# Performance work log

Measured on AMD Instinct MI355X. Metric: run time of the kernel, lower is better.

The kernel has to match this reference:

```python
import jax, jax.numpy as jnp
import numpy as np

B, L, D, H, E, M, P = 2, 512, 768, 12, 32, 4, 256
EMB, BS, MAP, C = 768, 64, 256, 97


def setup_inputs() -> dict:
    key = jax.random.key(0)
    ks = jax.random.split(key, 16)
    w = lambda k, s: (0.02 * jax.random.normal(k, s, jnp.float32))
    seq = jax.random.normal(ks[0], (B, L, D), jnp.float32)
    attn = jax.random.uniform(ks[1], (B, H, L, L), jnp.float32)
    entity_pos = jax.random.randint(ks[2], (B, E, M), 0, L - 2)
    # distinct (h, t) entity pairs per document -> unique mention-pair scatter slots
    grid = jnp.stack(jnp.meshgrid(jnp.arange(E), jnp.arange(E), indexing='ij'), -1).reshape(-1, 2)
    hts = jnp.stack([grid[jax.random.permutation(jax.random.fold_in(ks[3], b), E * E)[:P]] for b in range(B)], 0)
    mention_idx = jnp.broadcast_to(jnp.arange(E * M).reshape(E, M), (B, E, M))
    return {
        'seq': seq, 'attn': attn,
        'entity_pos': entity_pos, 'hts': hts, 'mention_idx': mention_idx,
        'W_head': w(ks[4], (2 * D, EMB)), 'b_head': jnp.zeros((EMB,), jnp.float32),
        'W_tail': w(ks[5], (2 * D, EMB)), 'b_tail': jnp.zeros((EMB,), jnp.float32),
        'W_rel': w(ks[6], (EMB * BS, C)), 'b_rel': jnp.zeros((C,), jnp.float32),
        'W_fh': w(ks[7], (D, EMB)), 'W_ft': w(ks[8], (D, EMB)), 'b_f': jnp.zeros((EMB,), jnp.float32),
        'W_unet': w(ks[9], (EMB, C)), 'b_unet': jnp.zeros((C,), jnp.float32),
        'W_mlp': w(ks[10], (EMB, C)), 'b_mlp': jnp.zeros((C,), jnp.float32),
        'W_bil': w(ks[11], (3 * C, C)), 'b_bil': jnp.zeros((C,), jnp.float32),
    }


def reference(seq, attn, entity_pos, hts, mention_idx,
              W_head, b_head, W_tail, b_tail, W_rel, b_rel,
              W_fh, W_ft, b_f, W_unet, b_unet, W_mlp, b_mlp, W_bil, b_bil):
    pos = entity_pos + 1                                 # bert offset
    b3 = jnp.arange(B)[:, None, None]
    ment_emb = seq[b3, pos]                              # [B,E,M,D] mention gather
    ment_att = attn[b3, :, pos]                          # [B,E,M,H,L]
    ent_emb = jax.nn.logsumexp(ment_emb, axis=2)         # [B,E,D] logsumexp pool
    ent_att = ment_att.mean(axis=2)                      # [B,E,H,L]
    b2 = jnp.arange(B)[:, None]
    h_idx, t_idx = hts[..., 0], hts[..., 1]
    hs, ts = ent_emb[b2, h_idx], ent_emb[b2, t_idx]      # [B,P,D]
    ha, ta = ent_att[b2, h_idx], ent_att[b2, t_idx]      # [B,P,H,L]
    ht_att = (ha * ta).mean(2)                           # [B,P,L]
    ht_att = ht_att / (ht_att.sum(-1, keepdims=True) + 1e-5)
    rs = jnp.einsum('bld,bpl->bpd', seq, ht_att)         # localized context
    N = B * P
    hz = jnp.tanh(jnp.concatenate([hs, rs], -1).reshape(N, 2 * D) @ W_head + b_head)
    tz = jnp.tanh(jnp.concatenate([ts, rs], -1).reshape(N, 2 * D) @ W_tail + b_tail)
    bl = (hz.reshape(N, EMB // BS, BS, 1) * tz.reshape(N, EMB // BS, 1, BS)).reshape(N, EMB * BS)
    r1 = bl @ W_rel + b_rel                              # [N,C]
    # mention-pair dense map scatter (map_rss)
    ment_flat = ment_emb.reshape(B, E * M, D)
    mh = mention_idx[b2, h_idx]                          # [B,P,M]
    mt = mention_idx[b2, t_idx]
    mh2 = jnp.broadcast_to(mh[:, :, :, None], (B, P, M, M))
    mt2 = jnp.broadcast_to(mt[:, :, None, :], (B, P, M, M))
    b4 = jnp.broadcast_to(jnp.arange(B)[:, None, None, None], (B, P, M, M))
    eh = ment_flat[b4, mh2]                              # [B,P,M,M,D]
    et = ment_flat[b4, mt2]
    feat = eh @ W_fh + et @ W_ft + b_f                   # fused Linear(cat(h,t))
    mp = jnp.zeros((B, MAP, MAP, EMB), seq.dtype).at[b4, mh2, mt2].set(feat)
    enc2 = jnp.tanh(mp @ W_unet + b_unet)                # UNet-channel surrogate
    enc3 = jax.nn.gelu(mp @ W_mlp + b_mlp)               # MLP-channel surrogate
    r2 = jax.nn.logsumexp(enc2[b4, mh2, mt2], axis=(2, 3)).reshape(N, C)
    r3 = jax.nn.logsumexp(enc3[b4, mh2, mt2], axis=(2, 3)).reshape(N, C)
    return jnp.concatenate([r1, r2, r3], -1) @ W_bil + b_bil
```

## Files before the change

kernel.cpp:

```cpp
#include <hip/hip_runtime.h>
#include <hip/hip_bf16.h>

#define B_  2
#define L_  512
#define D_  768
#define H_  12
#define E_  32
#define M_  4
#define P_  256
#define EMB_ 768
#define BS_ 64
#define C_  97
#define N_  (B_*P_)

#define KTOT_    49152
#define CPAD_    112
#define KSPLIT_  48
#define KCHUNK_  (KTOT_/KSPLIT_)
#define PSTR_    128
#define TILE_    (CPAD_*64)

typedef __hip_bfloat16 bf16;
typedef __attribute__((ext_vector_type(8))) short bf16x8;
typedef __attribute__((ext_vector_type(4))) float f32x4;
typedef __attribute__((ext_vector_type(8))) float f32x8;

__device__ inline float ldIn(const void* p, long idx, int isbf) {
    return isbf ? (float)((const bf16*)p)[idx] : ((const float*)p)[idx];
}

__device__ inline unsigned short f2bf(float f) {
    bf16 h = (bf16)f;
    return *(unsigned short*)&h;
}

__device__ inline float bf2f(unsigned short u) {
    bf16 h = *(bf16*)&u;
    return (float)h;
}

__global__ void dtype_detect(const void* __restrict__ seq, int* __restrict__ flag,
                             float* __restrict__ c23) {
    __shared__ int cnt;
    if (threadIdx.x == 0) cnt = 0;
    if (threadIdx.x < 2*C_) c23[threadIdx.x] = 0.f;
    __syncthreads();
    const unsigned short* u = (const unsigned short*)seq;
    int bad = 0;
    for (int i = threadIdx.x; i < 1024; i += 256) {
        unsigned short e = (u[i] >> 7) & 0xFF;
        if (e >= 140) bad++;
    }
    atomicAdd(&cnt, bad);
    __syncthreads();
    if (threadIdx.x == 0) flag[0] = (cnt < 16) ? 1 : 0;
}

struct PrepArgs {
    const void* src[8];
    long off[8];
    int K[8];
    int Ncols[8];
    int Npad[8];
    unsigned short* dst[8];
    const void* W_bil;  float* W_bilF;
    const void* b_f; const void* W_unet; const void* b_unet;
    const void* W_mlp; const void* b_mlp; float* c23;
    const void* W_rel; unsigned short* WBt;
};

union PrepSm {
    float T[32][65];
    unsigned short TW[CPAD_][72];
};

__global__ void prep_kernel(PrepArgs a, const int* __restrict__ dtf) {
    int isbf = dtf[0];
    int z = blockIdx.z;
    __shared__ PrepSm sm;
    int tid = threadIdx.x;
    if (z == 0) {
        int lin = blockIdx.y*48 + blockIdx.x;
        if (lin >= 96) return;
        int c = tid;
        if (c >= C_) return;
        float s2 = 0.f, s3 = 0.f;
        int d0 = lin*8;
        for (int i = 0; i < 8; i++) {
            int d = d0 + i;
            float bf = ldIn(a.b_f, d, isbf);
            s2 += bf * ldIn(a.W_unet, (long)d*C_ + c, isbf);
            s3 += bf * ldIn(a.W_mlp,  (long)d*C_ + c, isbf);
        }
        if (lin == 0) {
            s2 += ldIn(a.b_unet, c, isbf);
            s3 += ldIn(a.b_mlp,  c, isbf);
        }
        atomicAdd(&a.c23[c], s2);
        atomicAdd(&a.c23[C_ + c], s3);
    } else if (z == 1) {
        int lin = blockIdx.y*48 + blockIdx.x;
        if (lin >= KTOT_/64) return;
        int k0 = lin * 64;
        for (int idx = tid; idx < 64*97; idx += 256) {
            int kk = idx / 97, c = idx % 97;
            sm.TW[c][kk] = f2bf(ldIn(a.W_rel, (long)(k0+kk)*C_ + c, isbf));
        }
        for (int idx = tid; idx < 15*64; idx += 256) {
            sm.TW[97 + (idx>>6)][idx & 63] = 0;
        }
        __syncthreads();
        unsigned short* tb = a.WBt + (long)lin*TILE_;
        for (int t = 0; t < 4; t++) {
            int idx = tid + t*256;
            if (idx < 896) {
                int l  = idx & 63;
                int h  = (idx >> 6) & 1;
                int ct = idx >> 7;
                int row = ct*16 + (l & 15);
                int col = h*32 + (l >> 4)*8;
                *(uint4*)(tb + idx*8) = *(uint4*)&sm.TW[row][col];
            }
        }
    } else if (z <= 9) {
        int j = z - 2;
        int K = a.K[j], Ncols = a.Ncols[j], Npad = a.Npad[j];
        int k0 = blockIdx.x*32, n0 = blockIdx.y*64;
        if (k0 >= K || n0 >= Npad) return;
        const void* src = a.src[j];
        long off = a.off[j];
        unsigned short* dst = a.dst[j];
        int c64 = tid & 63, r4 = tid >> 6;
        for (int p = 0; p < 8; p++) {
            int r = r4 + p*4;
            int n = n0 + c64;
            sm.T[r][c64] = (n < Ncols) ? ldIn(src, off + (long)(k0+r)*Ncols + n, isbf) : 0.f;
        }
        __syncthreads();
        int cc = tid & 31, n8 = tid >> 5;
        for (int p = 0; p < 8; p++) {
            int nn = n8 + p*8;
            dst[(long)(n0+nn)*K + k0 + cc] = f2bf(sm.T[cc][nn]);
        }
    } else {
        int lin = blockIdx.y*48 + blockIdx.x;
        int idx = lin*256 + tid;
        if (idx < 291*C_) a.W_bilF[idx] = ldIn(a.W_bil, idx, isbf);
    }
}

__global__ void gather_kernel(const void* __restrict__ seq, const void* __restrict__ attn,
                              const int* __restrict__ entity_pos,
                              unsigned short* __restrict__ mentb, float* __restrict__ ent_emb,
                              float* __restrict__ ent_att, const int* __restrict__ dtf) {
    int isbf = dtf[0];
    if (blockIdx.x < 768) {
        int beh = blockIdx.x;
        int h = beh % H_;
        int be = beh / H_;
        int b = be >> 5;
        int pos[M_];
        for (int m = 0; m < M_; m++) pos[m] = entity_pos[be*M_+m] + 1;
        for (int l = threadIdx.x; l < L_; l += 256) {
            float s = 0.f;
            for (int m = 0; m < M_; m++)
                s += ldIn(attn, (((long)(b*H_ + h))*L_ + pos[m])*L_ + l, isbf);
            ent_att[(long)beh*L_ + l] = 0.25f * s;
        }
    } else {
        int be = blockIdx.x - 768;
        int b = be >> 5;
        int pos[M_];
        for (int m = 0; m < M_; m++) pos[m] = entity_pos[be*M_+m] + 1;
        for (int d = threadIdx.x; d < D_; d += 256) {
            float x[M_];
            for (int m = 0; m < M_; m++) {
                x[m] = ldIn(seq, ((long)b*L_ + pos[m])*D_ + d, isbf);
                mentb[((long)be*M_ + m)*D_ + d] = f2bf(x[m]);
            }
            float mx = fmaxf(fmaxf(x[0],x[1]), fmaxf(x[2],x[3]));
            float s = expf(x[0]-mx)+expf(x[1]-mx)+expf(x[2]-mx)+expf(x[3]-mx);
            ent_emb[(long)be*D_ + d] = mx + logf(s);
        }
    }
}

__global__ void htatt_kernel(const float* __restrict__ ent_att, const int* __restrict__ hts,
                             unsigned short* __restrict__ htb) {
    int bp = blockIdx.x;
    int b = bp >> 8;
    int h_e = hts[bp*2+0], t_e = hts[bp*2+1];
    const float* ea_h = ent_att + (long)((b*E_ + h_e)*H_)*L_;
    const float* ea_t = ent_att + (long)((b*E_ + t_e)*H_)*L_;
    __shared__ float red[256];
    float v[2];
    for (int t = 0; t < 2; t++) {
        int l = threadIdx.x + t*256;
        float s = 0.f;
        for (int h = 0; h < H_; h++) s += ea_h[h*L_+l] * ea_t[h*L_+l];
        v[t] = s * (1.0f/H_);
    }
    red[threadIdx.x] = v[0] + v[1];
    __syncthreads();
    for (int off = 128; off > 0; off >>= 1) {
        if (threadIdx.x < off) red[threadIdx.x] += red[threadIdx.x+off];
        __syncthreads();
    }
    float inv = 1.0f / (red[0] + 1e-5f);
    for (int t = 0; t < 2; t++) {
        int l = threadIdx.x + t*256;
        htb[(long)bp*L_ + l] = f2bf(v[t] * inv);
    }
}

__global__ void catb_kernel(const float* __restrict__ ent_emb, const float* __restrict__ rs,
                            const int* __restrict__ hts,
                            unsigned short* __restrict__ hcatb, unsigned short* __restrict__ tcatb) {
    int n = blockIdx.x;
    int b = n >> 8;
    int h_e = hts[n*2+0], t_e = hts[n*2+1];
    const float* eh = ent_emb + (long)(b*E_ + h_e)*D_;
    const float* et = ent_emb + (long)(b*E_ + t_e)*D_;
    const float* r  = rs + (long)n*D_;
    for (int k = threadIdx.x; k < D_; k += 256) {
        hcatb[(long)n*1536 + k] = f2bf(eh[k]);
        tcatb[(long)n*1536 + k] = f2bf(et[k]);
        unsigned short rb = f2bf(r[k]);
        hcatb[(long)n*1536 + 768 + k] = rb;
        tcatb[(long)n*1536 + 768 + k] = rb;
    }
}

struct MfmaJob {
    const unsigned short* A[4];
    const unsigned short* Bt[4];
    const void* bias[4];
    void* C[4];
    int K[4];
    int ldc[4];
    int act[4];
    int obf[4];
};

__global__ void mfma_nt2_kernel(MfmaJob args, const int* __restrict__ dtf) {
    int z = blockIdx.z;
    const unsigned short* A  = args.A[z];
    const unsigned short* Bt = args.Bt[z];
    const void* bias = args.bias[z];
    void* C = args.C[z];
    int K = args.K[z], ldc = args.ldc[z], act = args.act[z], obf = args.obf[z];
    __shared__ unsigned short Al[2][32][72];
    __shared__ unsigned short Btl[2][32][72];
    int m0 = blockIdx.x*32, n0 = blockIdx.y*32;
    int tid = threadIdx.x, wave = tid>>6, lane = tid&63;
    int lm = lane&15, lq = lane>>4;
    int rowg = wave>>1, cgrp = wave&1;
    int rr = tid >> 3;
    int kc = (tid & 7) * 8;
    uint4 ra, rb;

    ra = *(const uint4*)(A  + (long)(m0+rr)*K + kc);
    rb = *(const uint4*)(Bt + (long)(n0+rr)*K + kc);
    *(uint4*)&Al[0][rr][kc]  = ra;
    *(uint4*)&Btl[0][rr][kc] = rb;

    int nst = K >> 6;
    f32x4 acc = {};
    for (int ks = 0; ks < nst; ks++) {
        __syncthreads();
        if (ks+1 < nst) {
            int k0 = (ks+1) << 6;
            ra = *(const uint4*)(A  + (long)(m0+rr)*K + k0 + kc);
            rb = *(const uint4*)(Bt + (long)(n0+rr)*K + k0 + kc);
        }
        int cb = ks & 1;
        #pragma unroll
        for (int half = 0; half < 2; half++) {
            bf16x8 af  = *(bf16x8*)&Al[cb][rowg*16+lm][half*32+lq*8];
            bf16x8 bfr = *(bf16x8*)&Btl[cb][cgrp*16+lm][half*32+lq*8];
            acc = __builtin_amdgcn_mfma_f32_16x16x32_bf16(af, bfr, acc, 0, 0, 0);
        }
        if (ks+1 < nst) {
            int nb = (ks+1) & 1;
            *(uint4*)&Al[nb][rr][kc]  = ra;
            *(uint4*)&Btl[nb][rr][kc] = rb;
        }
    }
    int isbf = dtf[0];
    int n = n0 + cgrp*16 + lm;
    float bia = bias ? ldIn(bias, n, isbf) : 0.f;
    #pragma unroll
    for (int r = 0; r < 4; r++) {
        int m = m0 + rowg*16 + lq*4 + r;
        float v = acc[r] + bia;
        if (act == 1) v = tanhf(v);
        if (obf) ((unsigned short*)C)[(long)m*ldc + n] = f2bf(v);
        else     ((float*)C)[(long)m*ldc + n] = v;
    }
}

__global__ __launch_bounds__(256, 3)
void r1_mfma_kernel(const float* __restrict__ hz, const float* __restrict__ tz,
                    const unsigned short* __restrict__ WBt,
                    float* __restrict__ partial) {
    __shared__ float hzL[32][17];
    int kz = blockIdx.x;
    int nb0 = blockIdx.y * 32;
    int gk0 = kz * 16;
    int gi0 = kz * 16;
    int g0 = (kz * KCHUNK_) >> 12;
    int tid = threadIdx.x;
    int wave = tid >> 6, lane = tid & 63;
    int lm = lane & 15;
    int ctb = wave * 2;
    int nct = (wave < 3) ? 2 : 1;

    {
        int r = tid >> 3, q = (tid & 7) * 2;
        float2 v = *(const float2*)(hz + (long)(nb0 + r)*EMB_ + gi0 + q);
        hzL[r][q] = v.x; hzL[r][q+1] = v.y;
    }
    int lq = lane >> 4;
    f32x8 tza[2], tzb[2];
    #pragma unroll
    for (int rg = 0; rg < 2; rg++) {
        const float* tp = tz + (long)(nb0 + rg*16 + lm)*EMB_ + g0*64;
        float4 x0 = *(const float4*)(tp + lq*8);
        float4 y0 = *(const float4*)(tp + lq*8 + 4);
        float4 x1 = *(const float4*)(tp + 32 + lq*8);
        float4 y1 = *(const float4*)(tp + 32 + lq*8 + 4);
        tza[rg][0]=x0.x; tza[rg][1]=x0.y; tza[rg][2]=x0.z; tza[rg][3]=x0.w;
        tza[rg][4]=y0.x; tza[rg][5]=y0.y; tza[rg][6]=y0.z; tza[rg][7]=y0.w;
        tzb[rg][0]=x1.x; tzb[rg][1]=x1.y; tzb[rg][2]=x1.z; tzb[rg][3]=x1.w;
        tzb[rg][4]=y1.x; tzb[rg][5]=y1.y; tzb[rg][6]=y1.z; tzb[rg][7]=y1.w;
    }
    __syncthreads();

    const unsigned short* wb = WBt + (long)gk0*TILE_ + lane*8;

    f32x4 acc[2][2] = {};
    bf16x8 cb[2][2];
    #pragma unroll
    for (int ct = 0; ct < 2; ct++)
        if (ct < nct)
            #pragma unroll
            for (int h = 0; h < 2; h++)
                cb[ct][h] = *(const bf16x8*)(wb + ((ctb+ct)*2 + h)*512);

    #pragma unroll 2
    for (int ks = 0; ks < KCHUNK_/64; ks++) {
        bf16x8 nbuf[2][2];
        if (ks+1 < KCHUNK_/64) {
            const unsigned short* wn = wb + (long)(ks+1)*TILE_;
            #pragma unroll
            for (int ct = 0; ct < 2; ct++)
                if (ct < nct)
                    #pragma unroll
                    for (int h = 0; h < 2; h++)
                        nbuf[ct][h] = *(const bf16x8*)(wn + ((ctb+ct)*2 + h)*512);
        }
        float hv0 = hzL[lm][ks];
        float hv1 = hzL[16 + lm][ks];
        unsigned short o00[8], o01[8], o10[8], o11[8];
        #pragma unroll
        for (int e = 0; e < 8; e++) {
            o00[e] = f2bf(tza[0][e] * hv0);
            o01[e] = f2bf(tzb[0][e] * hv0);
            o10[e] = f2bf(tza[1][e] * hv1);
            o11[e] = f2bf(tzb[1][e] * hv1);
        }
        bf16x8 a00 = *(bf16x8*)o00, a01 = *(bf16x8*)o01;
        bf16x8 a10 = *(bf16x8*)o10, a11 = *(bf16x8*)o11;
        #pragma unroll
        for (int ct = 0; ct < 2; ct++) {
            if (ct < nct) {
                acc[ct][0] = __builtin_amdgcn_mfma_f32_16x16x32_bf16(a00, cb[ct][0], acc[ct][0], 0, 0, 0);
                acc[ct][0] = __builtin_amdgcn_mfma_f32_16x16x32_bf16(a01, cb[ct][1], acc[ct][0], 0, 0, 0);
                acc[ct][1] = __builtin_amdgcn_mfma_f32_16x16x32_bf16(a10, cb[ct][0], acc[ct][1], 0, 0, 0);
                acc[ct][1] = __builtin_amdgcn_mfma_f32_16x16x32_bf16(a11, cb[ct][1], acc[ct][1], 0, 0, 0);
            }
        }
        if (ks+1 < KCHUNK_/64) {
            #pragma unroll
            for (int ct = 0; ct < 2; ct++)
                if (ct < nct)
                    #pragma unroll
                    for (int h = 0; h < 2; h++)
                        cb[ct][h] = nbuf[ct][h];
        }
    }
    #pragma unroll
    for (int ct = 0; ct < 2; ct++) {
        if (ct < nct || wave == 3) {
            int c = (ctb + ct)*16 + lm;
            #pragma unroll
            for (int rg = 0; rg < 2; rg++) {
                #pragma unroll
                for (int r = 0; r < 4; r++) {
                    int nl = rg*16 + lq*4 + r;
                    float v = (ct < nct) ? acc[ct][rg][r] : 0.f;
                    partial[((long)(nb0+nl)*KSPLIT_ + kz)*PSTR_ + c] = v;
                }
            }
        }
    }
}

__global__ void r23out_kernel(const float* __restrict__ partial, const void* __restrict__ b_rel,
                              const float* __restrict__ mu, const float* __restrict__ c23,
                              const int* __restrict__ hts, const int* __restrict__ mention_idx,
                              const float* __restrict__ W_bilF, const void* __restrict__ b_bil,
                              void* __restrict__ out, const int* __restrict__ dtf) {
    int bp = blockIdx.x;
    int b = bp >> 8;
    int c = threadIdx.x;
    int isbf = dtf[0];
    __shared__ float row[292];
    if (c < C_) {
        const float* pr = partial + (long)bp*KSPLIT_*PSTR_;
        float r1v = 0.f;
        #pragma unroll 8
        for (int kz = 0; kz < KSPLIT_; kz++)
            r1v += pr[kz*PSTR_ + c];
        r1v += ldIn(b_rel, c, isbf);
        int h_e = hts[bp*2+0], t_e = hts[bp*2+1];
        const float* mu2h = mu;
        const float* mu2t = mu + 32768;
        const float* mu3h = mu + 65536;
        const float* mu3t = mu + 98304;
        float ah2[4], at2[4], ah3[4], at3[4];
        for (int m = 0; m < 4; m++) {
            int emh = mention_idx[(b*E_ + h_e)*M_ + m];
            int emt = mention_idx[(b*E_ + t_e)*M_ + m];
            ah2[m] = mu2h[(long)(b*128 + emh)*128 + c];
            ah3[m] = mu3h[(long)(b*128 + emh)*128 + c];
            at2[m] = mu2t[(long)(b*128 + emt)*128 + c];
            at3[m] = mu3t[(long)(b*128 + emt)*128 + c];
        }
        float c2 = c23[c], c3 = c23[C_ + c];
        float v2[16], v3[16];
        int q = 0;
        for (int i = 0; i < 4; i++) {
            for (int j = 0; j < 4; j++, q++) {
                float x2 = ah2[i] + at2[j] + c2;
                v2[q] = tanhf(x2);
                float x3 = ah3[i] + at3[j] + c3;
                float t = tanhf(0.7978845608028654f * (x3 + 0.044715f*x3*x3*x3));
                v3[q] = 0.5f * x3 * (1.0f + t);
            }
        }
        float m2 = v2[0], m3 = v3[0];
        for (q = 1; q < 16; q++) { m2 = fmaxf(m2, v2[q]); m3 = fmaxf(m3, v3[q]); }
        float s2 = 0.f, s3 = 0.f;
        for (q = 0; q < 16; q++) { s2 += expf(v2[q]-m2); s3 += expf(v3[q]-m3); }
        row[c]        = r1v;
        row[C_ + c]   = m2 + logf(s2);
        row[2*C_ + c] = m3 + logf(s3);
    }
    __syncthreads();
    if (c >= C_) return;
    float a0 = 0.f, a1 = 0.f, a2 = 0.f, a3 = 0.f;
    #pragma unroll 4
    for (int k = 0; k < 288; k += 4) {
        a0 += row[k+0] * W_bilF[(k+0)*C_ + c];
        a1 += row[k+1] * W_bilF[(k+1)*C_ + c];
        a2 += row[k+2] * W_bilF[(k+2)*C_ + c];
        a3 += row[k+3] * W_bilF[(k+3)*C_ + c];
    }
    a0 += row[288] * W_bilF[288*C_ + c];
    a1 += row[289] * W_bilF[289*C_ + c];
    a2 += row[290] * W_bilF[290*C_ + c];
    float v = a0 + a1 + a2 + a3 + ldIn(b_bil, c, isbf);
    if (isbf) ((bf16*)out)[(long)bp*C_ + c] = (bf16)v;
    else      ((float*)out)[(long)bp*C_ + c] = v;
}

extern "C" void kernel_launch(void* const* d_in, const int* in_sizes, int n_in,
                              void* d_out, int out_size, void* d_ws, size_t ws_size,
                              hipStream_t stream) {
    const void* seq        = d_in[0];
    const void* attn       = d_in[1];
    const int*  entity_pos = (const int*)d_in[2];
    const int*  hts        = (const int*)d_in[3];
    const int*  mention_idx= (const int*)d_in[4];
    const void* W_head     = d_in[5];
    const void* b_head     = d_in[6];
    const void* W_tail     = d_in[7];
    const void* b_tail     = d_in[8];
    const void* W_rel      = d_in[9];
    const void* b_rel      = d_in[10];
    const void* W_fh       = d_in[11];
    const void* W_ft       = d_in[12];
    const void* b_f        = d_in[13];
    const void* W_unet     = d_in[14];
    const void* b_unet     = d_in[15];
    const void* W_mlp      = d_in[16];
    const void* b_mlp      = d_in[17];
    const void* W_bil      = d_in[18];
    const void* b_bil      = d_in[19];

    float* w = (float*)d_ws;
    int*   dtf      = (int*)w;
    unsigned short* mentb = (unsigned short*)(w + 64);
    float* ent_emb  = w + 98368;
    float* ent_att  = w + 147520;
    unsigned short* htb = (unsigned short*)(w + 540736);
    float* rs       = w + 671808;
    float* hz       = w + 1065024;
    float* tz       = w + 1458240;
    float* mu       = w + 1851456;
    float* c23      = w + 1982528;
    unsigned short* seqT  = (unsigned short*)(w + 1982784);
    unsigned short* WhT   = (unsigned short*)(w + 2376000);
    unsigned short* WtT   = (unsigned short*)(w + 2965824);
    unsigned short* WfhT  = (unsigned short*)(w + 3555648);
    unsigned short* WftT  = (unsigned short*)(w + 3850560);
    unsigned short* WunetT= (unsigned short*)(w + 4145472);
    unsigned short* WmlpT = (unsigned short*)(w + 4194624);
    unsigned short* Tbh   = (unsigned short*)(w + 4243776);
    unsigned short* Tbt   = (unsigned short*)(w + 4342080);
    unsigned short* hcatb = (unsigned short*)(w + 4440384);
    unsigned short* tcatb = (unsigned short*)(w + 4833600);
    unsigned short* WBt   = (unsigned short*)(w + 5226816);
    float* partial  = w + 7979328;
    float* W_bilF   = w + 11649344;

    dtype_detect<<<1, 256, 0, stream>>>(seq, dtf, c23);
    {
        PrepArgs a = {};
        const void* srcs[8] = {W_head, W_tail, W_fh, W_ft, W_unet, W_mlp, seq, seq};
        long offs[8]   = {0,0,0,0,0,0,0,393216};
        int Ks[8]      = {1536,1536,768,768,768,768,512,512};
        int Ncols8[8]  = {768,768,768,768,97,97,768,768};
        int Npads[8]   = {768,768,768,768,128,128,768,768};
        unsigned short* dsts[8] = {WhT, WtT, WfhT, WftT, WunetT, WmlpT, seqT, seqT+393216};
        for (int z = 0; z < 8; z++) {
            a.src[z]=srcs[z]; a.off[z]=offs[z]; a.K[z]=Ks[z];
            a.Ncols[z]=Ncols8[z]; a.Npad[z]=Npads[z]; a.dst[z]=dsts[z];
        }
        a.W_bil = W_bil; a.W_bilF = W_bilF;
        a.b_f = b_f; a.W_unet = W_unet; a.b_unet = b_unet;
        a.W_mlp = W_mlp; a.b_mlp = b_mlp; a.c23 = c23;
        a.W_rel = W_rel; a.WBt = WBt;
        prep_kernel<<<dim3(48, 16, 11), 256, 0, stream>>>(a, dtf);
    }
    gather_kernel<<<768 + 64, 256, 0, stream>>>(seq, attn, entity_pos, mentb, ent_emb, ent_att, dtf);
    htatt_kernel<<<N_, 256, 0, stream>>>(ent_att, hts, htb);
    {
        MfmaJob ga = {};
        for (int z = 0; z < 2; z++) {
            ga.A[z] = htb + (long)z*256*512; ga.Bt[z] = seqT + (long)z*393216;
            ga.bias[z] = nullptr; ga.C[z] = rs + (long)z*256*768;
            ga.K[z] = 512; ga.ldc[z] = 768; ga.act[z] = 0; ga.obf[z] = 0;
        }
        ga.A[2] = mentb; ga.Bt[2] = WfhT; ga.bias[2] = nullptr; ga.C[2] = Tbh;
        ga.K[2] = 768; ga.ldc[2] = 768; ga.act[2] = 0; ga.obf[2] = 1;
        ga.A[3] = mentb; ga.Bt[3] = WftT; ga.bias[3] = nullptr; ga.C[3] = Tbt;
        ga.K[3] = 768; ga.ldc[3] = 768; ga.act[3] = 0; ga.obf[3] = 1;
        mfma_nt2_kernel<<<dim3(8, 24, 4), 256, 0, stream>>>(ga, dtf);
    }
    catb_kernel<<<N_, 256, 0, stream>>>(ent_emb, rs, hts, hcatb, tcatb);
    {
        MfmaJob ga = {};
        ga.A[0] = hcatb; ga.Bt[0] = WhT; ga.bias[0] = b_head; ga.C[0] = hz;
        ga.A[1] = tcatb; ga.Bt[1] = WtT; ga.bias[1] = b_tail; ga.C[1] = tz;
        for (int z = 0; z < 2; z++) { ga.K[z] = 1536; ga.ldc[z] = 768; ga.act[z] = 1; ga.obf[z] = 0; }
        mfma_nt2_kernel<<<dim3(16, 24, 2), 256, 0, stream>>>(ga, dtf);
    }
    {
        MfmaJob ga = {};
        const unsigned short* As[4] = {Tbh, Tbt, Tbh, Tbt};
        const unsigned short* Bs[4] = {WunetT, WunetT, WmlpT, WmlpT};
        for (int q = 0; q < 4; q++) {
            ga.A[q] = As[q]; ga.Bt[q] = Bs[q]; ga.bias[q] = nullptr;
            ga.C[q] = mu + q*32768;
            ga.K[q] = 768; ga.ldc[q] = 128; ga.act[q] = 0; ga.obf[q] = 0;
        }
        mfma_nt2_kernel<<<dim3(8, 4, 4), 256, 0, stream>>>(ga, dtf);
    }
    r1_mfma_kernel<<<dim3(KSPLIT_, 16), 256, 0, stream>>>(hz, tz, WBt, partial);
    r23out_kernel<<<N_, 128, 0, stream>>>(partial, b_rel, mu, c23, hts, mention_idx,
                                          W_bilF, b_bil, d_out, dtf);
}
```

Measured before the change: 218.0 us.

## Fuse dtype detection, entity attention and pair attention; merge small GEMM launches

Drops the separate dtype_detect kernel; each kernel now detects dtype inline with a wave ballot over the first 64 elements of seq. The entity attention averaging and the head/tail attention product are fused into one kernel that reads attn rows directly per pair, so the ent_att intermediate goes away. The c23 bias reduction now writes 16 partials instead of using atomics, which also removes the need to zero the buffer first. The two trailing small GEMM launches are merged into one launch with per-job bounds. This removes launches and intermediate traffic but recomputes attention gathers per pair, and the dtype check now samples fewer elements.

```diff
diff --git a/kernel.cpp b/kernel.cpp
--- a/kernel.cpp
+++ b/kernel.cpp
@@ -34,26 +34,12 @@
     return *(unsigned short*)&h;
 }
 
-__device__ inline float bf2f(unsigned short u) {
-    bf16 h = *(bf16*)&u;
-    return (float)h;
-}
-
-__global__ void dtype_detect(const void* __restrict__ seq, int* __restrict__ flag,
-                             float* __restrict__ c23) {
-    __shared__ int cnt;
-    if (threadIdx.x == 0) cnt = 0;
-    if (threadIdx.x < 2*C_) c23[threadIdx.x] = 0.f;
-    __syncthreads();
-    const unsigned short* u = (const unsigned short*)seq;
-    int bad = 0;
-    for (int i = threadIdx.x; i < 1024; i += 256) {
-        unsigned short e = (u[i] >> 7) & 0xFF;
-        if (e >= 140) bad++;
-    }
-    atomicAdd(&cnt, bad);
-    __syncthreads();
-    if (threadIdx.x == 0) flag[0] = (cnt < 16) ? 1 : 0;
+__device__ inline int detect_bf(const void* seqd) {
+    const unsigned short* u = (const unsigned short*)seqd;
+    int lane = threadIdx.x & 63;
+    unsigned short e = (u[lane] >> 7) & 0xFF;
+    unsigned long long m = __ballot(e >= 140);
+    return m == 0ull;
 }
 
 struct PrepArgs {
@@ -65,8 +51,9 @@
     unsigned short* dst[8];
     const void* W_bil;  float* W_bilF;
     const void* b_f; const void* W_unet; const void* b_unet;
-    const void* W_mlp; const void* b_mlp; float* c23;
+    const void* W_mlp; const void* b_mlp; float* c23p;
     const void* W_rel; unsigned short* WBt;
+    const void* seqd;
 };
 
 union PrepSm {
@@ -74,19 +61,19 @@
     unsigned short TW[CPAD_][72];
 };
 
-__global__ void prep_kernel(PrepArgs a, const int* __restrict__ dtf) {
-    int isbf = dtf[0];
+__global__ void prep_kernel(PrepArgs a) {
+    int isbf = detect_bf(a.seqd);
     int z = blockIdx.z;
     __shared__ PrepSm sm;
     int tid = threadIdx.x;
     if (z == 0) {
         int lin = blockIdx.y*48 + blockIdx.x;
-        if (lin >= 96) return;
+        if (lin >= 16) return;
         int c = tid;
         if (c >= C_) return;
         float s2 = 0.f, s3 = 0.f;
-        int d0 = lin*8;
-        for (int i = 0; i < 8; i++) {
+        int d0 = lin*48;
+        for (int i = 0; i < 48; i++) {
             int d = d0 + i;
             float bf = ldIn(a.b_f, d, isbf);
             s2 += bf * ldIn(a.W_unet, (long)d*C_ + c, isbf);
@@ -96,8 +83,8 @@
             s2 += ldIn(a.b_unet, c, isbf);
             s3 += ldIn(a.b_mlp,  c, isbf);
         }
-        atomicAdd(&a.c23[c], s2);
-        atomicAdd(&a.c23[C_ + c], s3);
+        a.c23p[lin*194 + c]      = s2;
+        a.c23p[lin*194 + 97 + c] = s3;
     } else if (z == 1) {
         int lin = blockIdx.y*48 + blockIdx.x;
         if (lin >= KTOT_/64) return;
@@ -149,26 +136,49 @@
     }
 }
 
-__global__ void gather_kernel(const void* __restrict__ seq, const void* __restrict__ attn,
-                              const int* __restrict__ entity_pos,
-                              unsigned short* __restrict__ mentb, float* __restrict__ ent_emb,
-                              float* __restrict__ ent_att, const int* __restrict__ dtf) {
-    int isbf = dtf[0];
-    if (blockIdx.x < 768) {
-        int beh = blockIdx.x;
-        int h = beh % H_;
-        int be = beh / H_;
-        int b = be >> 5;
-        int pos[M_];
-        for (int m = 0; m < M_; m++) pos[m] = entity_pos[be*M_+m] + 1;
-        for (int l = threadIdx.x; l < L_; l += 256) {
+__global__ void ghatt_kernel(const void* __restrict__ seq, const void* __restrict__ attn,
+                             const int* __restrict__ entity_pos, const int* __restrict__ hts,
+                             unsigned short* __restrict__ mentb, float* __restrict__ ent_emb,
+                             unsigned short* __restrict__ htb) {
+    int isbf = detect_bf(seq);
+    if (blockIdx.x < 512) {
+        int bp = blockIdx.x;
+        int b = bp >> 8;
+        int h_e = hts[bp*2+0], t_e = hts[bp*2+1];
+        int ph[M_], pt[M_];
+        for (int m = 0; m < M_; m++) {
+            ph[m] = entity_pos[(b*E_ + h_e)*M_ + m] + 1;
+            pt[m] = entity_pos[(b*E_ + t_e)*M_ + m] + 1;
+        }
+        __shared__ float red[256];
+        float v[2];
+        for (int t = 0; t < 2; t++) {
+            int l = threadIdx.x + t*256;
             float s = 0.f;
-            for (int m = 0; m < M_; m++)
-                s += ldIn(attn, (((long)(b*H_ + h))*L_ + pos[m])*L_ + l, isbf);
-            ent_att[(long)beh*L_ + l] = 0.25f * s;
+            for (int h = 0; h < H_; h++) {
+                long hb = ((long)(b*H_ + h))*L_;
+                float ha = 0.f, ta = 0.f;
+                for (int m = 0; m < M_; m++) {
+                    ha += ldIn(attn, (hb + ph[m])*L_ + l, isbf);
+                    ta += ldIn(attn, (hb + pt[m])*L_ + l, isbf);
+                }
+                s += ha * ta;
+            }
+            v[t] = s * (0.0625f / H_);
+        }
+        red[threadIdx.x] = v[0] + v[1];
+        __syncthreads();
+        for (int off = 128; off > 0; off >>= 1) {
+            if (threadIdx.x < off) red[threadIdx.x] += red[threadIdx.x+off];
+            __syncthreads();
+        }
+        float inv = 1.0f / (red[0] + 1e-5f);
+        for (int t = 0; t < 2; t++) {
+            int l = threadIdx.x + t*256;
+            htb[(long)bp*L_ + l] = f2bf(v[t] * inv);
         }
     } else {
-        int be = blockIdx.x - 768;
+        int be = blockIdx.x - 512;
         int b = be >> 5;
         int pos[M_];
         for (int m = 0; m < M_; m++) pos[m] = entity_pos[be*M_+m] + 1;
@@ -182,34 +192,6 @@
             float s = expf(x[0]-mx)+expf(x[1]-mx)+expf(x[2]-mx)+expf(x[3]-mx);
             ent_emb[(long)be*D_ + d] = mx + logf(s);
         }
-    }
-}
-
-__global__ void htatt_kernel(const float* __restrict__ ent_att, const int* __restrict__ hts,
-                             unsigned short* __restrict__ htb) {
-    int bp = blockIdx.x;
-    int b = bp >> 8;
-    int h_e = hts[bp*2+0], t_e = hts[bp*2+1];
-    const float* ea_h = ent_att + (long)((b*E_ + h_e)*H_)*L_;
-    const float* ea_t = ent_att + (long)((b*E_ + t_e)*H_)*L_;
-    __shared__ float red[256];
-    float v[2];
-    for (int t = 0; t < 2; t++) {
-        int l = threadIdx.x + t*256;
-        float s = 0.f;
-        for (int h = 0; h < H_; h++) s += ea_h[h*L_+l] * ea_t[h*L_+l];
-        v[t] = s * (1.0f/H_);
-    }
-    red[threadIdx.x] = v[0] + v[1];
-    __syncthreads();
-    for (int off = 128; off > 0; off >>= 1) {
-        if (threadIdx.x < off) red[threadIdx.x] += red[threadIdx.x+off];
-        __syncthreads();
-    }
-    float inv = 1.0f / (red[0] + 1e-5f);
-    for (int t = 0; t < 2; t++) {
-        int l = threadIdx.x + t*256;
-        htb[(long)bp*L_ + l] = f2bf(v[t] * inv);
     }
 }
 
@@ -232,18 +214,24 @@
 }
 
 struct MfmaJob {
-    const unsigned short* A[4];
-    const unsigned short* Bt[4];
-    const void* bias[4];
-    void* C[4];
-    int K[4];
-    int ldc[4];
-    int act[4];
-    int obf[4];
+    const unsigned short* A[8];
+    const unsigned short* Bt[8];
+    const void* bias[8];
+    void* C[8];
+    const void* seqd;
+    int K[8];
+    int ldc[8];
+    int act[8];
+    int obf[8];
+    int Mt[8];
+    int Nt[8];
 };
 
-__global__ void mfma_nt2_kernel(MfmaJob args, const int* __restrict__ dtf) {
+__global__ void mfma_nt2_kernel(MfmaJob args) {
     int z = blockIdx.z;
+    int m0 = blockIdx.x*32, n0 = blockIdx.y*32;
+    if (m0 >= args.Mt[z] || n0 >= args.Nt[z]) return;
+    int isbf = detect_bf(args.seqd);
     const unsigned short* A  = args.A[z];
     const unsigned short* Bt = args.Bt[z];
     const void* bias = args.bias[z];
@@ -251,7 +239,6 @@
     int K = args.K[z], ldc = args.ldc[z], act = args.act[z], obf = args.obf[z];
     __shared__ unsigned short Al[2][32][72];
     __shared__ unsigned short Btl[2][32][72];
-    int m0 = blockIdx.x*32, n0 = blockIdx.y*32;
     int tid = threadIdx.x, wave = tid>>6, lane = tid&63;
     int lm = lane&15, lq = lane>>4;
     int rowg = wave>>1, cgrp = wave&1;
@@ -286,7 +273,6 @@
             *(uint4*)&Btl[nb][rr][kc] = rb;
         }
     }
-    int isbf = dtf[0];
     int n = n0 + cgrp*16 + lm;
     float bia = bias ? ldIn(bias, n, isbf) : 0.f;
     #pragma unroll
@@ -407,14 +393,14 @@
 }
 
 __global__ void r23out_kernel(const float* __restrict__ partial, const void* __restrict__ b_rel,
-                              const float* __restrict__ mu, const float* __restrict__ c23,
+                              const float* __restrict__ mu, const float* __restrict__ c23p,
                               const int* __restrict__ hts, const int* __restrict__ mention_idx,
                               const float* __restrict__ W_bilF, const void* __restrict__ b_bil,
-                              void* __restrict__ out, const int* __restrict__ dtf) {
+                              void* __restrict__ out, const void* __restrict__ seqd) {
     int bp = blockIdx.x;
     int b = bp >> 8;
     int c = threadIdx.x;
-    int isbf = dtf[0];
+    int isbf = detect_bf(seqd);
     __shared__ float row[292];
     if (c < C_) {
         const float* pr = partial + (long)bp*KSPLIT_*PSTR_;
@@ -437,7 +423,12 @@
             at2[m] = mu2t[(long)(b*128 + emt)*128 + c];
             at3[m] = mu3t[(long)(b*128 + emt)*128 + c];
         }
-        float c2 = c23[c], c3 = c23[C_ + c];
+        float c2 = 0.f, c3 = 0.f;
+        #pragma unroll
+        for (int j = 0; j < 16; j++) {
+            c2 += c23p[j*194 + c];
+            c3 += c23p[j*194 + 97 + c];
+        }
         float v2[16], v3[16];
         int q = 0;
         for (int i = 0; i < 4; i++) {
@@ -500,16 +491,13 @@
     const void* b_bil      = d_in[19];
 
     float* w = (float*)d_ws;
-    int*   dtf      = (int*)w;
     unsigned short* mentb = (unsigned short*)(w + 64);
     float* ent_emb  = w + 98368;
-    float* ent_att  = w + 147520;
     unsigned short* htb = (unsigned short*)(w + 540736);
     float* rs       = w + 671808;
     float* hz       = w + 1065024;
     float* tz       = w + 1458240;
     float* mu       = w + 1851456;
-    float* c23      = w + 1982528;
     unsigned short* seqT  = (unsigned short*)(w + 1982784);
     unsigned short* WhT   = (unsigned short*)(w + 2376000);
     unsigned short* WtT   = (unsigned short*)(w + 2965824);
@@ -523,9 +511,9 @@
     unsigned short* tcatb = (unsigned short*)(w + 4833600);
     unsigned short* WBt   = (unsigned short*)(w + 5226816);
     float* partial  = w + 7979328;
+    float* c23p     = w + 11200000;
     float* W_bilF   = w + 11649344;
 
-    dtype_detect<<<1, 256, 0, stream>>>(seq, dtf, c23);
     {
         PrepArgs a = {};
         const void* srcs[8] = {W_head, W_tail, W_fh, W_ft, W_unet, W_mlp, seq, seq};
@@ -540,45 +528,51 @@
         }
         a.W_bil = W_bil; a.W_bilF = W_bilF;
         a.b_f = b_f; a.W_unet = W_unet; a.b_unet = b_unet;
-        a.W_mlp = W_mlp; a.b_mlp = b_mlp; a.c23 = c23;
+        a.W_mlp = W_mlp; a.b_mlp = b_mlp; a.c23p = c23p;
         a.W_rel = W_rel; a.WBt = WBt;
-        prep_kernel<<<dim3(48, 16, 11), 256, 0, stream>>>(a, dtf);
-    }
-    gather_kernel<<<768 + 64, 256, 0, stream>>>(seq, attn, entity_pos, mentb, ent_emb, ent_att, dtf);
-    htatt_kernel<<<N_, 256, 0, stream>>>(ent_att, hts, htb);
+        a.seqd = seq;
+        prep_kernel<<<dim3(48, 16, 11), 256, 0, stream>>>(a);
+    }
+    ghatt_kernel<<<512 + 64, 256, 0, stream>>>(seq, attn, entity_pos, hts, mentb, ent_emb, htb);
     {
         MfmaJob ga = {};
+        ga.seqd = seq;
         for (int z = 0; z < 2; z++) {
             ga.A[z] = htb + (long)z*256*512; ga.Bt[z] = seqT + (long)z*393216;
             ga.bias[z] = nullptr; ga.C[z] = rs + (long)z*256*768;
             ga.K[z] = 512; ga.ldc[z] = 768; ga.act[z] = 0; ga.obf[z] = 0;
+            ga.Mt[z] = 256; ga.Nt[z] = 768;
         }
         ga.A[2] = mentb; ga.Bt[2] = WfhT; ga.bias[2] = nullptr; ga.C[2] = Tbh;
         ga.K[2] = 768; ga.ldc[2] = 768; ga.act[2] = 0; ga.obf[2] = 1;
+        ga.Mt[2] = 256; ga.Nt[2] = 768;
         ga.A[3] = mentb; ga.Bt[3] = WftT; ga.bias[3] = nullptr; ga.C[3] = Tbt;
         ga.K[3] = 768; ga.ldc[3] = 768; ga.act[3] = 0; ga.obf[3] = 1;
-        mfma_nt2_kernel<<<dim3(8, 24, 4), 256, 0, stream>>>(ga, dtf);
+        ga.Mt[3] = 256; ga.Nt[3] = 768;
+        mfma_nt2_kernel<<<dim3(8, 24, 4), 256, 0, stream>>>(ga);
     }
     catb_kernel<<<N_, 256, 0, stream>>>(ent_emb, rs, hts, hcatb, tcatb);
     {
         MfmaJob ga = {};
+        ga.seqd = seq;
         ga.A[0] = hcatb; ga.Bt[0] = WhT; ga.bias[0] = b_head; ga.C[0] = hz;
         ga.A[1] = tcatb; ga.Bt[1] = WtT; ga.bias[1] = b_tail; ga.C[1] = tz;
-        for (int z = 0; z < 2; z++) { ga.K[z] = 1536; ga.ldc[z] = 768; ga.act[z] = 1; ga.obf[z] = 0; }
-        mfma_nt2_kernel<<<dim3(16, 24, 2), 256, 0, stream>>>(ga, dtf);
-    }
-    {
-        MfmaJob ga = {};
+        for (int z = 0; z < 2; z++) {
+            ga.K[z] = 1536; ga.ldc[z] = 768; ga.act[z] = 1; ga.obf[z] = 0;
+            ga.Mt[z] = 512; ga.Nt[z] = 768;
+        }
         const unsigned short* As[4] = {Tbh, Tbt, Tbh, Tbt};
         const unsigned short* Bs[4] = {WunetT, WunetT, WmlpT, WmlpT};
         for (int q = 0; q < 4; q++) {
-            ga.A[q] = As[q]; ga.Bt[q] = Bs[q]; ga.bias[q] = nullptr;
-            ga.C[q] = mu + q*32768;
-            ga.K[q] = 768; ga.ldc[q] = 128; ga.act[q] = 0; ga.obf[q] = 0;
-        }
-        mfma_nt2_kernel<<<dim3(8, 4, 4), 256, 0, stream>>>(ga, dtf);
+            int z = 2 + q;
+            ga.A[z] = As[q]; ga.Bt[z] = Bs[q]; ga.bias[z] = nullptr;
+            ga.C[z] = mu + q*32768;
+            ga.K[z] = 768; ga.ldc[z] = 128; ga.act[z] = 0; ga.obf[z] = 0;
+            ga.Mt[z] = 256; ga.Nt[z] = 128;
+        }
+        mfma_nt2_kernel<<<dim3(16, 24, 6), 256, 0, stream>>>(ga);
     }
     r1_mfma_kernel<<<dim3(KSPLIT_, 16), 256, 0, stream>>>(hz, tz, WBt, partial);
-    r23out_kernel<<<N_, 128, 0, stream>>>(partial, b_rel, mu, c23, hts, mention_idx,
-                                          W_bilF, b_bil, d_out, dtf);
-}
+    r23out_kernel<<<N_, 128, 0, stream>>>(partial, b_rel, mu, c23p, hts, mention_idx,
+                                          W_bilF, b_bil, d_out, seq);
+}
```

Result: no change. 215.7 us (-1.0%).
